# Kernel tuning notes

Hardware: AMD Instinct MI355X
Metric: run time of the kernel (lower is better)

Reference implementation:

```python
import jax, jax.numpy as jnp
import numpy as np

BS, OBJ, D = 32, 128, 256
R, E = 32, 64          # max_rels, relation_embedding_size
DEPTH = 3


def setup_inputs() -> dict:
    key = jax.random.key(0)
    ks = jax.random.split(key, 8)
    x = jax.random.normal(ks[0], (BS, OBJ, D), dtype=jnp.float32)
    # adjacency-style aggregation matrix [batch, objects, max_rels*objects]
    A = jax.random.uniform(ks[1], (BS, OBJ, R * OBJ), dtype=jnp.float32)
    rel_table = jax.random.normal(ks[2], (R, E), dtype=jnp.float32)
    # per-depth linear params (torch Linear y = x @ W^T + b; we store W already transposed to [in,out])
    s1 = 1.0 / np.sqrt(D)
    s2 = 1.0 / np.sqrt(D + E)
    W1 = jax.random.uniform(ks[3], (DEPTH, D, D), jnp.float32, -s1, s1)
    b1 = jax.random.uniform(ks[4], (DEPTH, D), jnp.float32, -s1, s1)
    W2 = jax.random.uniform(ks[5], (DEPTH, D + E, D), jnp.float32, -s2, s2)
    b2 = jax.random.uniform(ks[6], (DEPTH, D), jnp.float32, -s2, s2)
    return {"x": x, "A": A, "rel_table": rel_table, "W1": W1, "b1": b1, "W2": W2, "b2": b2}


def reference(x, A, rel_table, W1, b1, W2, b2):
    bs, o, d = x.shape
    r, e = rel_table.shape
    depth = W1.shape[0]
    # relation embeddings tiled per object (object-major, rel-minor): [o*r, e]
    rel = jnp.tile(rel_table, (o, 1))
    rel_b = jnp.broadcast_to(rel, (bs, o * r, e))
    for i in range(depth):
        # repeat each object's features over all relations: [bs, o*r, d]
        xr = jnp.repeat(x, r, axis=1)
        xr = jnp.concatenate([xr, rel_b], axis=-1)            # [bs, o*r, d+e]
        h1 = jnp.einsum('bod,df->bof', x, W1[i]) + b1[i]       # self transform
        h2 = jnp.einsum('bnc,cf->bnf', xr, W2[i]) + b2[i]      # relation-augmented transform
        agg = jnp.einsum('bon,bnf->bof', A, h2)                # bmm aggregate
        x = jnp.tanh(h1 + agg + x)                             # residual + tanh
    return x
```

## Files before the change

### kernel.cpp

```cpp
#include <hip/hip_runtime.h>
#include <math.h>

#define BS 32
#define OBJ 128
#define DD 256
#define RR 32
#define EE 64
#define NDEPTH 3

__global__ __launch_bounds__(256) void k_reduceA(const float* __restrict__ A,
                                                 float* __restrict__ Ao,
                                                 float* __restrict__ Ar,
                                                 float* __restrict__ As) {
    int wave = threadIdx.x >> 6;
    int lane = threadIdx.x & 63;
    int row  = blockIdx.x * 4 + wave;
    const float4* src = (const float4*)(A + (size_t)row * (RR * OBJ));
    float* AoRow = Ao + (size_t)row * OBJ;

    float4 arAcc = make_float4(0.f, 0.f, 0.f, 0.f);
#pragma unroll
    for (int it = 0; it < 16; ++it) {
        float4 v = src[it * 64 + lane];
        arAcc.x += v.x; arAcc.y += v.y; arAcc.z += v.z; arAcc.w += v.w;
        float s = v.x + v.y + v.z + v.w;
        s += __shfl_xor(s, 1);
        s += __shfl_xor(s, 2);
        s += __shfl_xor(s, 4);
        if ((lane & 7) == 0) AoRow[it * 8 + (lane >> 3)] = s;
    }
#pragma unroll
    for (int m = 8; m <= 32; m <<= 1) {
        arAcc.x += __shfl_xor(arAcc.x, m);
        arAcc.y += __shfl_xor(arAcc.y, m);
        arAcc.z += __shfl_xor(arAcc.z, m);
        arAcc.w += __shfl_xor(arAcc.w, m);
    }
    if (lane < 8) ((float4*)(Ar + (size_t)row * RR))[lane] = arAcc;
    float t = arAcc.x + arAcc.y + arAcc.z + arAcc.w;
    t += __shfl_xor(t, 1);
    t += __shfl_xor(t, 2);
    t += __shfl_xor(t, 4);
    if (lane == 0) As[row] = t;
}

__global__ __launch_bounds__(256) void k_rel(const float* __restrict__ rel,
                                             const float* __restrict__ W2,
                                             float* __restrict__ relpart) {
    int dr = blockIdx.x;
    int d = dr >> 5, r = dr & 31;
    int f = threadIdx.x;
    const float* w  = W2 + (size_t)d * (DD + EE) * DD + (size_t)DD * DD;
    const float* rl = rel + (size_t)r * EE;
    float acc = 0.f;
#pragma unroll 8
    for (int e = 0; e < EE; ++e)
        acc = fmaf(rl[e], w[(size_t)e * DD + f], acc);
    relpart[(size_t)dr * DD + f] = acc;
}

__global__ __launch_bounds__(256) void k_gemm1(const float* __restrict__ X,
                                               const float* __restrict__ W1,
                                               const float* __restrict__ W2,
                                               const float* __restrict__ b1,
                                               int d,
                                               float* __restrict__ h1,
                                               float* __restrict__ xw) {
    __shared__ float Xs[64][33];
    __shared__ float Ws[32][64];

    int m0 = blockIdx.y * 64;
    int n0blk = blockIdx.x * 64;
    bool isW1 = (n0blk < 256);
    int ncol0 = isW1 ? n0blk : (n0blk - 256);
    const float* Wbase = isW1 ? (W1 + (size_t)d * DD * DD)
                              : (W2 + (size_t)d * (DD + EE) * DD);

    int tid = threadIdx.x;
    int tx = tid & 15;
    int ty = tid >> 4;
    float acc[4][4] = {};

    for (int k0 = 0; k0 < 256; k0 += 32) {
#pragma unroll
        for (int i = 0; i < 2; ++i) {
            int idx = tid + 256 * i;
            int rrow = idx >> 3, c4 = idx & 7;
            float4 v = *(const float4*)(X + (size_t)(m0 + rrow) * DD + k0 + c4 * 4);
            Xs[rrow][c4 * 4 + 0] = v.x; Xs[rrow][c4 * 4 + 1] = v.y;
            Xs[rrow][c4 * 4 + 2] = v.z; Xs[rrow][c4 * 4 + 3] = v.w;
        }
#pragma unroll
        for (int i = 0; i < 2; ++i) {
            int idx = tid + 256 * i;
            int rrow = idx >> 4, c4 = idx & 15;
            *(float4*)(&Ws[rrow][c4 * 4]) =
                *(const float4*)(Wbase + (size_t)(k0 + rrow) * DD + ncol0 + c4 * 4);
        }
        __syncthreads();
#pragma unroll
        for (int kk = 0; kk < 32; ++kk) {
            float a0 = Xs[ty * 4 + 0][kk];
            float a1 = Xs[ty * 4 + 1][kk];
            float a2 = Xs[ty * 4 + 2][kk];
            float a3 = Xs[ty * 4 + 3][kk];
            float4 bv = *(const float4*)(&Ws[kk][tx * 4]);
            acc[0][0] = fmaf(a0, bv.x, acc[0][0]);
            acc[0][1] = fmaf(a0, bv.y, acc[0][1]);
            acc[0][2] = fmaf(a0, bv.z, acc[0][2]);
            acc[0][3] = fmaf(a0, bv.w, acc[0][3]);
            acc[1][0] = fmaf(a1, bv.x, acc[1][0]);
            acc[1][1] = fmaf(a1, bv.y, acc[1][1]);
            acc[1][2] = fmaf(a1, bv.z, acc[1][2]);
            acc[1][3] = fmaf(a1, bv.w, acc[1][3]);
            acc[2][0] = fmaf(a2, bv.x, acc[2][0]);
            acc[2][1] = fmaf(a2, bv.y, acc[2][1]);
            acc[2][2] = fmaf(a2, bv.z, acc[2][2]);
            acc[2][3] = fmaf(a2, bv.w, acc[2][3]);
            acc[3][0] = fmaf(a3, bv.x, acc[3][0]);
            acc[3][1] = fmaf(a3, bv.y, acc[3][1]);
            acc[3][2] = fmaf(a3, bv.z, acc[3][2]);
            acc[3][3] = fmaf(a3, bv.w, acc[3][3]);
        }
        __syncthreads();
    }

    float4 bias = make_float4(0.f, 0.f, 0.f, 0.f);
    if (isW1) bias = *(const float4*)(b1 + (size_t)d * DD + ncol0 + tx * 4);
    float* dst = isW1 ? h1 : xw;
#pragma unroll
    for (int i = 0; i < 4; ++i) {
        float4 o;
        o.x = acc[i][0] + bias.x;
        o.y = acc[i][1] + bias.y;
        o.z = acc[i][2] + bias.z;
        o.w = acc[i][3] + bias.w;
        *(float4*)(dst + (size_t)(m0 + ty * 4 + i) * DD + ncol0 + tx * 4) = o;
    }
}

__global__ __launch_bounds__(256) void k_agg(const float* __restrict__ Ao,
                                             const float* __restrict__ Ar,
                                             const float* __restrict__ As,
                                             const float* __restrict__ relpart,
                                             const float* __restrict__ b2,
                                             int d,
                                             const float* __restrict__ xw,
                                             const float* __restrict__ h1,
                                             const float* __restrict__ xin,
                                             float* __restrict__ xout) {
    __shared__ float Asm[64][33];
    __shared__ float Bs[32][64];

    int b  = blockIdx.z;
    int m0 = blockIdx.y * 64;
    int n0 = blockIdx.x * 64;
    int tid = threadIdx.x;
    int tx = tid & 15, ty = tid >> 4;

    const float* AoB = Ao + ((size_t)b * OBJ + m0) * OBJ;
    const float* ArB = Ar + ((size_t)b * OBJ + m0) * RR;
    const float* xwB = xw + (size_t)b * OBJ * DD;
    const float* rp  = relpart + (size_t)d * RR * DD;

    float acc[4][4] = {};

    for (int t = 0; t < 5; ++t) {
        if (t < 4) {
            int k0 = t * 32;
#pragma unroll
            for (int i = 0; i < 2; ++i) {
                int idx = tid + 256 * i;
                int rr = idx >> 3, c4 = idx & 7;
                float4 v = *(const float4*)(AoB + (size_t)rr * OBJ + k0 + c4 * 4);
                Asm[rr][c4 * 4 + 0] = v.x; Asm[rr][c4 * 4 + 1] = v.y;
                Asm[rr][c4 * 4 + 2] = v.z; Asm[rr][c4 * 4 + 3] = v.w;
            }
#pragma unroll
            for (int i = 0; i < 2; ++i) {
                int idx = tid + 256 * i;
                int rr = idx >> 4, c4 = idx & 15;
                *(float4*)(&Bs[rr][c4 * 4]) =
                    *(const float4*)(xwB + (size_t)(k0 + rr) * DD + n0 + c4 * 4);
            }
        } else {
#pragma unroll
            for (int i = 0; i < 2; ++i) {
                int idx = tid + 256 * i;
                int rr = idx >> 3, c4 = idx & 7;
                float4 v = *(const float4*)(ArB + (size_t)rr * RR + c4 * 4);
                Asm[rr][c4 * 4 + 0] = v.x; Asm[rr][c4 * 4 + 1] = v.y;
                Asm[rr][c4 * 4 + 2] = v.z; Asm[rr][c4 * 4 + 3] = v.w;
            }
#pragma unroll
            for (int i = 0; i < 2; ++i) {
                int idx = tid + 256 * i;
                int rr = idx >> 4, c4 = idx & 15;
                *(float4*)(&Bs[rr][c4 * 4]) =
                    *(const float4*)(rp + (size_t)rr * DD + n0 + c4 * 4);
            }
        }
        __syncthreads();
#pragma unroll
        for (int kk = 0; kk < 32; ++kk) {
            float a0 = Asm[ty * 4 + 0][kk];
            float a1 = Asm[ty * 4 + 1][kk];
            float a2 = Asm[ty * 4 + 2][kk];
            float a3 = Asm[ty * 4 + 3][kk];
            float4 bv = *(const float4*)(&Bs[kk][tx * 4]);
            acc[0][0] = fmaf(a0, bv.x, acc[0][0]);
            acc[0][1] = fmaf(a0, bv.y, acc[0][1]);
            acc[0][2] = fmaf(a0, bv.z, acc[0][2]);
            acc[0][3] = fmaf(a0, bv.w, acc[0][3]);
            acc[1][0] = fmaf(a1, bv.x, acc[1][0]);
            acc[1][1] = fmaf(a1, bv.y, acc[1][1]);
            acc[1][2] = fmaf(a1, bv.z, acc[1][2]);
            acc[1][3] = fmaf(a1, bv.w, acc[1][3]);
            acc[2][0] = fmaf(a2, bv.x, acc[2][0]);
            acc[2][1] = fmaf(a2, bv.y, acc[2][1]);
            acc[2][2] = fmaf(a2, bv.z, acc[2][2]);
            acc[2][3] = fmaf(a2, bv.w, acc[2][3]);
            acc[3][0] = fmaf(a3, bv.x, acc[3][0]);
            acc[3][1] = fmaf(a3, bv.y, acc[3][1]);
            acc[3][2] = fmaf(a3, bv.z, acc[3][2]);
            acc[3][3] = fmaf(a3, bv.w, acc[3][3]);
        }
        __syncthreads();
    }

    float4 b2v = *(const float4*)(b2 + (size_t)d * DD + n0 + tx * 4);
#pragma unroll
    for (int i = 0; i < 4; ++i) {
        int m = m0 + ty * 4 + i;
        float asv = As[(size_t)b * OBJ + m];
        size_t base = ((size_t)b * OBJ + m) * DD + n0 + tx * 4;
        float4 hv = *(const float4*)(h1 + base);
        float4 xv = *(const float4*)(xin + base);
        float4 o;
        o.x = tanhf(acc[i][0] + asv * b2v.x + hv.x + xv.x);
        o.y = tanhf(acc[i][1] + asv * b2v.y + hv.y + xv.y);
        o.z = tanhf(acc[i][2] + asv * b2v.z + hv.z + xv.z);
        o.w = tanhf(acc[i][3] + asv * b2v.w + hv.w + xv.w);
        *(float4*)(xout + base) = o;
    }
}

extern "C" void kernel_launch(void* const* d_in, const int* in_sizes, int n_in,
                              void* d_out, int out_size, void* d_ws, size_t ws_size,
                              hipStream_t stream) {
    const float* x    = (const float*)d_in[0];
    const float* A    = (const float*)d_in[1];
    const float* rel  = (const float*)d_in[2];
    const float* W1   = (const float*)d_in[3];
    const float* b1   = (const float*)d_in[4];
    const float* W2   = (const float*)d_in[5];
    const float* b2   = (const float*)d_in[6];
    float* out = (float*)d_out;

    float* Ao      = (float*)d_ws;
    float* Ar      = Ao + (size_t)BS * OBJ * OBJ;
    float* As_     = Ar + (size_t)BS * OBJ * RR;
    float* relpart = As_ + (size_t)BS * OBJ;
    float* xwbuf   = relpart + (size_t)NDEPTH * RR * DD;
    float* h1buf   = xwbuf + (size_t)BS * OBJ * DD;
    float* xbuf    = h1buf + (size_t)BS * OBJ * DD;

    k_reduceA<<<dim3(BS * OBJ / 4), dim3(256), 0, stream>>>(A, Ao, Ar, As_);
    k_rel<<<dim3(NDEPTH * RR), dim3(256), 0, stream>>>(rel, W2, relpart);

    const float* xcur = x;
    for (int d = 0; d < NDEPTH; ++d) {
        float* xnext = (d == NDEPTH - 1) ? out : xbuf;
        k_gemm1<<<dim3(8, 64), dim3(256), 0, stream>>>(xcur, W1, W2, b1, d, h1buf, xwbuf);
        k_agg<<<dim3(4, 2, BS), dim3(256), 0, stream>>>(Ao, Ar, As_, relpart, b2, d,
                                                        xwbuf, h1buf, xcur, xnext);
        xcur = xnext;
    }
}
```

Before: 214.6 us.

## Double-buffer shared tiles with register prefetch and transposed A layout in GEMM kernels

Both k_gemm1 and k_agg now stage tiles through registers into double-buffered shared memory. The next k-slice is loaded while the current one is computed, which leaves one barrier per iteration instead of two. The A/X operand is stored transposed so each thread reads a float4 of four rows per k step instead of four scalar loads. k_gemm1 also widens its tile to 64x128 (8 outputs per thread) and halves its grid, which raises register pressure and cuts the number of blocks to 256.

```diff
diff --git a/kernel.cpp b/kernel.cpp
--- a/kernel.cpp
+++ b/kernel.cpp
@@ -66,76 +66,109 @@
                                                int d,
                                                float* __restrict__ h1,
                                                float* __restrict__ xw) {
-    __shared__ float Xs[64][33];
-    __shared__ float Ws[32][64];
-
-    int m0 = blockIdx.y * 64;
-    int n0blk = blockIdx.x * 64;
-    bool isW1 = (n0blk < 256);
-    int ncol0 = isW1 ? n0blk : (n0blk - 256);
+    __shared__ float XT[2][32][68];
+    __shared__ float Ws[2][32][132];
+
+    const int m0 = blockIdx.y * 64;
+    const int n0blk = blockIdx.x * 128;
+    const bool isW1 = (n0blk < 256);
+    const int ncol0 = isW1 ? n0blk : (n0blk - 256);
     const float* Wbase = isW1 ? (W1 + (size_t)d * DD * DD)
                               : (W2 + (size_t)d * (DD + EE) * DD);
 
-    int tid = threadIdx.x;
-    int tx = tid & 15;
-    int ty = tid >> 4;
-    float acc[4][4] = {};
-
-    for (int k0 = 0; k0 < 256; k0 += 32) {
-#pragma unroll
-        for (int i = 0; i < 2; ++i) {
-            int idx = tid + 256 * i;
-            int rrow = idx >> 3, c4 = idx & 7;
-            float4 v = *(const float4*)(X + (size_t)(m0 + rrow) * DD + k0 + c4 * 4);
-            Xs[rrow][c4 * 4 + 0] = v.x; Xs[rrow][c4 * 4 + 1] = v.y;
-            Xs[rrow][c4 * 4 + 2] = v.z; Xs[rrow][c4 * 4 + 3] = v.w;
-        }
-#pragma unroll
-        for (int i = 0; i < 2; ++i) {
-            int idx = tid + 256 * i;
-            int rrow = idx >> 4, c4 = idx & 15;
-            *(float4*)(&Ws[rrow][c4 * 4]) =
-                *(const float4*)(Wbase + (size_t)(k0 + rrow) * DD + ncol0 + c4 * 4);
-        }
-        __syncthreads();
+    const int tid = threadIdx.x;
+    const int tx = tid & 15;
+    const int ty = tid >> 4;
+
+    const int xm0 = tid >> 3;
+    const int xc  = tid & 7;
+    const int wr0 = tid >> 5;
+    const int wc  = tid & 31;
+
+    float4 xr[2], wr4[4];
+    float acc0[4][4] = {};
+    float acc1[4][4] = {};
+
+#pragma unroll
+    for (int i = 0; i < 2; ++i)
+        xr[i] = *(const float4*)(X + (size_t)(m0 + xm0 + 32 * i) * DD + xc * 4);
+#pragma unroll
+    for (int i = 0; i < 4; ++i)
+        wr4[i] = *(const float4*)(Wbase + (size_t)(wr0 + 8 * i) * DD + ncol0 + wc * 4);
+#pragma unroll
+    for (int i = 0; i < 2; ++i) {
+        XT[0][xc * 4 + 0][xm0 + 32 * i] = xr[i].x;
+        XT[0][xc * 4 + 1][xm0 + 32 * i] = xr[i].y;
+        XT[0][xc * 4 + 2][xm0 + 32 * i] = xr[i].z;
+        XT[0][xc * 4 + 3][xm0 + 32 * i] = xr[i].w;
+    }
+#pragma unroll
+    for (int i = 0; i < 4; ++i)
+        *(float4*)(&Ws[0][wr0 + 8 * i][wc * 4]) = wr4[i];
+    __syncthreads();
+
+    for (int t = 0; t < 8; ++t) {
+        const int cur = t & 1;
+        if (t < 7) {
+            const int k0 = (t + 1) * 32;
+#pragma unroll
+            for (int i = 0; i < 2; ++i)
+                xr[i] = *(const float4*)(X + (size_t)(m0 + xm0 + 32 * i) * DD + k0 + xc * 4);
+#pragma unroll
+            for (int i = 0; i < 4; ++i)
+                wr4[i] = *(const float4*)(Wbase + (size_t)(k0 + wr0 + 8 * i) * DD + ncol0 + wc * 4);
+        }
 #pragma unroll
         for (int kk = 0; kk < 32; ++kk) {
-            float a0 = Xs[ty * 4 + 0][kk];
-            float a1 = Xs[ty * 4 + 1][kk];
-            float a2 = Xs[ty * 4 + 2][kk];
-            float a3 = Xs[ty * 4 + 3][kk];
-            float4 bv = *(const float4*)(&Ws[kk][tx * 4]);
-            acc[0][0] = fmaf(a0, bv.x, acc[0][0]);
-            acc[0][1] = fmaf(a0, bv.y, acc[0][1]);
-            acc[0][2] = fmaf(a0, bv.z, acc[0][2]);
-            acc[0][3] = fmaf(a0, bv.w, acc[0][3]);
-            acc[1][0] = fmaf(a1, bv.x, acc[1][0]);
-            acc[1][1] = fmaf(a1, bv.y, acc[1][1]);
-            acc[1][2] = fmaf(a1, bv.z, acc[1][2]);
-            acc[1][3] = fmaf(a1, bv.w, acc[1][3]);
-            acc[2][0] = fmaf(a2, bv.x, acc[2][0]);
-            acc[2][1] = fmaf(a2, bv.y, acc[2][1]);
-            acc[2][2] = fmaf(a2, bv.z, acc[2][2]);
-            acc[2][3] = fmaf(a2, bv.w, acc[2][3]);
-            acc[3][0] = fmaf(a3, bv.x, acc[3][0]);
-            acc[3][1] = fmaf(a3, bv.y, acc[3][1]);
-            acc[3][2] = fmaf(a3, bv.z, acc[3][2]);
-            acc[3][3] = fmaf(a3, bv.w, acc[3][3]);
-        }
-        __syncthreads();
-    }
-
-    float4 bias = make_float4(0.f, 0.f, 0.f, 0.f);
-    if (isW1) bias = *(const float4*)(b1 + (size_t)d * DD + ncol0 + tx * 4);
+            float4 a  = *(const float4*)(&XT[cur][kk][ty * 4]);
+            float4 b0 = *(const float4*)(&Ws[cur][kk][tx * 4]);
+            float4 b1v = *(const float4*)(&Ws[cur][kk][64 + tx * 4]);
+            const float am[4] = {a.x, a.y, a.z, a.w};
+#pragma unroll
+            for (int i = 0; i < 4; ++i) {
+                acc0[i][0] = fmaf(am[i], b0.x, acc0[i][0]);
+                acc0[i][1] = fmaf(am[i], b0.y, acc0[i][1]);
+                acc0[i][2] = fmaf(am[i], b0.z, acc0[i][2]);
+                acc0[i][3] = fmaf(am[i], b0.w, acc0[i][3]);
+                acc1[i][0] = fmaf(am[i], b1v.x, acc1[i][0]);
+                acc1[i][1] = fmaf(am[i], b1v.y, acc1[i][1]);
+                acc1[i][2] = fmaf(am[i], b1v.z, acc1[i][2]);
+                acc1[i][3] = fmaf(am[i], b1v.w, acc1[i][3]);
+            }
+        }
+        if (t < 7) {
+            const int nxt = cur ^ 1;
+#pragma unroll
+            for (int i = 0; i < 2; ++i) {
+                XT[nxt][xc * 4 + 0][xm0 + 32 * i] = xr[i].x;
+                XT[nxt][xc * 4 + 1][xm0 + 32 * i] = xr[i].y;
+                XT[nxt][xc * 4 + 2][xm0 + 32 * i] = xr[i].z;
+                XT[nxt][xc * 4 + 3][xm0 + 32 * i] = xr[i].w;
+            }
+#pragma unroll
+            for (int i = 0; i < 4; ++i)
+                *(float4*)(&Ws[nxt][wr0 + 8 * i][wc * 4]) = wr4[i];
+            __syncthreads();
+        }
+    }
+
+    float4 bias0 = make_float4(0.f, 0.f, 0.f, 0.f);
+    float4 bias1 = bias0;
+    if (isW1) {
+        bias0 = *(const float4*)(b1 + (size_t)d * DD + ncol0 + tx * 4);
+        bias1 = *(const float4*)(b1 + (size_t)d * DD + ncol0 + 64 + tx * 4);
+    }
     float* dst = isW1 ? h1 : xw;
 #pragma unroll
     for (int i = 0; i < 4; ++i) {
-        float4 o;
-        o.x = acc[i][0] + bias.x;
-        o.y = acc[i][1] + bias.y;
-        o.z = acc[i][2] + bias.z;
-        o.w = acc[i][3] + bias.w;
-        *(float4*)(dst + (size_t)(m0 + ty * 4 + i) * DD + ncol0 + tx * 4) = o;
+        size_t base = (size_t)(m0 + ty * 4 + i) * DD + ncol0;
+        float4 o0, o1;
+        o0.x = acc0[i][0] + bias0.x; o0.y = acc0[i][1] + bias0.y;
+        o0.z = acc0[i][2] + bias0.z; o0.w = acc0[i][3] + bias0.w;
+        o1.x = acc1[i][0] + bias1.x; o1.y = acc1[i][1] + bias1.y;
+        o1.z = acc1[i][2] + bias1.z; o1.w = acc1[i][3] + bias1.w;
+        *(float4*)(dst + base + tx * 4) = o0;
+        *(float4*)(dst + base + 64 + tx * 4) = o1;
     }
 }
 
@@ -149,83 +182,86 @@
                                              const float* __restrict__ h1,
                                              const float* __restrict__ xin,
                                              float* __restrict__ xout) {
-    __shared__ float Asm[64][33];
-    __shared__ float Bs[32][64];
-
-    int b  = blockIdx.z;
-    int m0 = blockIdx.y * 64;
-    int n0 = blockIdx.x * 64;
-    int tid = threadIdx.x;
-    int tx = tid & 15, ty = tid >> 4;
+    __shared__ float AT[2][32][68];
+    __shared__ float Bs[2][32][68];
+
+    const int b  = blockIdx.z;
+    const int m0 = blockIdx.y * 64;
+    const int n0 = blockIdx.x * 64;
+    const int tid = threadIdx.x;
+    const int tx = tid & 15, ty = tid >> 4;
 
     const float* AoB = Ao + ((size_t)b * OBJ + m0) * OBJ;
     const float* ArB = Ar + ((size_t)b * OBJ + m0) * RR;
     const float* xwB = xw + (size_t)b * OBJ * DD;
     const float* rp  = relpart + (size_t)d * RR * DD;
 
+    const int am0 = tid >> 3;
+    const int ac  = tid & 7;
+    const int br0 = tid >> 4;
+    const int bc  = tid & 15;
+
+    float4 areg[2], breg[2];
     float acc[4][4] = {};
 
+#pragma unroll
+    for (int i = 0; i < 2; ++i) {
+        areg[i] = *(const float4*)(AoB + (size_t)(am0 + 32 * i) * OBJ + ac * 4);
+        breg[i] = *(const float4*)(xwB + (size_t)(br0 + 16 * i) * DD + n0 + bc * 4);
+    }
+#pragma unroll
+    for (int i = 0; i < 2; ++i) {
+        AT[0][ac * 4 + 0][am0 + 32 * i] = areg[i].x;
+        AT[0][ac * 4 + 1][am0 + 32 * i] = areg[i].y;
+        AT[0][ac * 4 + 2][am0 + 32 * i] = areg[i].z;
+        AT[0][ac * 4 + 3][am0 + 32 * i] = areg[i].w;
+        *(float4*)(&Bs[0][br0 + 16 * i][bc * 4]) = breg[i];
+    }
+    __syncthreads();
+
     for (int t = 0; t < 5; ++t) {
+        const int cur = t & 1;
         if (t < 4) {
-            int k0 = t * 32;
+            if (t < 3) {
+                const int k0 = (t + 1) * 32;
+#pragma unroll
+                for (int i = 0; i < 2; ++i) {
+                    areg[i] = *(const float4*)(AoB + (size_t)(am0 + 32 * i) * OBJ + k0 + ac * 4);
+                    breg[i] = *(const float4*)(xwB + (size_t)(k0 + br0 + 16 * i) * DD + n0 + bc * 4);
+                }
+            } else {
+#pragma unroll
+                for (int i = 0; i < 2; ++i) {
+                    areg[i] = *(const float4*)(ArB + (size_t)(am0 + 32 * i) * RR + ac * 4);
+                    breg[i] = *(const float4*)(rp + (size_t)(br0 + 16 * i) * DD + n0 + bc * 4);
+                }
+            }
+        }
+#pragma unroll
+        for (int kk = 0; kk < 32; ++kk) {
+            float4 a = *(const float4*)(&AT[cur][kk][ty * 4]);
+            float4 bv = *(const float4*)(&Bs[cur][kk][tx * 4]);
+            const float am[4] = {a.x, a.y, a.z, a.w};
+#pragma unroll
+            for (int i = 0; i < 4; ++i) {
+                acc[i][0] = fmaf(am[i], bv.x, acc[i][0]);
+                acc[i][1] = fmaf(am[i], bv.y, acc[i][1]);
+                acc[i][2] = fmaf(am[i], bv.z, acc[i][2]);
+                acc[i][3] = fmaf(am[i], bv.w, acc[i][3]);
+            }
+        }
+        if (t < 4) {
+            const int nxt = cur ^ 1;
 #pragma unroll
             for (int i = 0; i < 2; ++i) {
-                int idx = tid + 256 * i;
-                int rr = idx >> 3, c4 = idx & 7;
-                float4 v = *(const float4*)(AoB + (size_t)rr * OBJ + k0 + c4 * 4);
-                Asm[rr][c4 * 4 + 0] = v.x; Asm[rr][c4 * 4 + 1] = v.y;
-                Asm[rr][c4 * 4 + 2] = v.z; Asm[rr][c4 * 4 + 3] = v.w;
-            }
-#pragma unroll
-            for (int i = 0; i < 2; ++i) {
-                int idx = tid + 256 * i;
-                int rr = idx >> 4, c4 = idx & 15;
-                *(float4*)(&Bs[rr][c4 * 4]) =
-                    *(const float4*)(xwB + (size_t)(k0 + rr) * DD + n0 + c4 * 4);
-            }
-        } else {
-#pragma unroll
-            for (int i = 0; i < 2; ++i) {
-                int idx = tid + 256 * i;
-                int rr = idx >> 3, c4 = idx & 7;
-                float4 v = *(const float4*)(ArB + (size_t)rr * RR + c4 * 4);
-                Asm[rr][c4 * 4 + 0] = v.x; Asm[rr][c4 * 4 + 1] = v.y;
-                Asm[rr][c4 * 4 + 2] = v.z; Asm[rr][c4 * 4 + 3] = v.w;
-            }
-#pragma unroll
-            for (int i = 0; i < 2; ++i) {
-                int idx = tid + 256 * i;
-                int rr = idx >> 4, c4 = idx & 15;
-                *(float4*)(&Bs[rr][c4 * 4]) =
-                    *(const float4*)(rp + (size_t)rr * DD + n0 + c4 * 4);
-            }
-        }
-        __syncthreads();
-#pragma unroll
-        for (int kk = 0; kk < 32; ++kk) {
-            float a0 = Asm[ty * 4 + 0][kk];
-            float a1 = Asm[ty * 4 + 1][kk];
-            float a2 = Asm[ty * 4 + 2][kk];
-            float a3 = Asm[ty * 4 + 3][kk];
-            float4 bv = *(const float4*)(&Bs[kk][tx * 4]);
-            acc[0][0] = fmaf(a0, bv.x, acc[0][0]);
-            acc[0][1] = fmaf(a0, bv.y, acc[0][1]);
-            acc[0][2] = fmaf(a0, bv.z, acc[0][2]);
-            acc[0][3] = fmaf(a0, bv.w, acc[0][3]);
-            acc[1][0] = fmaf(a1, bv.x, acc[1][0]);
-            acc[1][1] = fmaf(a1, bv.y, acc[1][1]);
-            acc[1][2] = fmaf(a1, bv.z, acc[1][2]);
-            acc[1][3] = fmaf(a1, bv.w, acc[1][3]);
-            acc[2][0] = fmaf(a2, bv.x, acc[2][0]);
-            acc[2][1] = fmaf(a2, bv.y, acc[2][1]);
-            acc[2][2] = fmaf(a2, bv.z, acc[2][2]);
-            acc[2][3] = fmaf(a2, bv.w, acc[2][3]);
-            acc[3][0] = fmaf(a3, bv.x, acc[3][0]);
-            acc[3][1] = fmaf(a3, bv.y, acc[3][1]);
-            acc[3][2] = fmaf(a3, bv.z, acc[3][2]);
-            acc[3][3] = fmaf(a3, bv.w, acc[3][3]);
-        }
-        __syncthreads();
+                AT[nxt][ac * 4 + 0][am0 + 32 * i] = areg[i].x;
+                AT[nxt][ac * 4 + 1][am0 + 32 * i] = areg[i].y;
+                AT[nxt][ac * 4 + 2][am0 + 32 * i] = areg[i].z;
+                AT[nxt][ac * 4 + 3][am0 + 32 * i] = areg[i].w;
+                *(float4*)(&Bs[nxt][br0 + 16 * i][bc * 4]) = breg[i];
+            }
+            __syncthreads();
+        }
     }
 
     float4 b2v = *(const float4*)(b2 + (size_t)d * DD + n0 + tx * 4);
@@ -271,7 +307,7 @@
     const float* xcur = x;
     for (int d = 0; d < NDEPTH; ++d) {
         float* xnext = (d == NDEPTH - 1) ? out : xbuf;
-        k_gemm1<<<dim3(8, 64), dim3(256), 0, stream>>>(xcur, W1, W2, b1, d, h1buf, xwbuf);
+        k_gemm1<<<dim3(4, 64), dim3(256), 0, stream>>>(xcur, W1, W2, b1, d, h1buf, xwbuf);
         k_agg<<<dim3(4, 2, BS), dim3(256), 0, stream>>>(Ao, Ar, As_, relpart, b2, d,
                                                         xwbuf, h1buf, xcur, xnext);
         xcur = xnext;
```

Result: slower. 258.4 us (+20.4%).

## Rewrite gemm1 as single-wave 8x8 register tile with double-buffered LDS

Applied to the files above, without the earlier changes.

The k_gemm1 tile GEMM now runs with 64 threads per block instead of 256, each computing an 8x8 output micro-tile, so fewer LDS reads are needed per FMA. Global loads for the next k-slice go into registers and are written to a second LDS buffer, which removes the __syncthreads barriers. The X tile uses an XOR-swizzled layout to avoid bank conflicts on float4 reads. With only 512 single-wave blocks, the GPU gets fewer waves to hide latency, and register pressure from 64 accumulators plus 16 prefetch float4s is high.

```diff
diff --git a/kernel.cpp b/kernel.cpp
--- a/kernel.cpp
+++ b/kernel.cpp
@@ -59,83 +59,108 @@
     relpart[(size_t)dr * DD + f] = acc;
 }
 
-__global__ __launch_bounds__(256) void k_gemm1(const float* __restrict__ X,
-                                               const float* __restrict__ W1,
-                                               const float* __restrict__ W2,
-                                               const float* __restrict__ b1,
-                                               int d,
-                                               float* __restrict__ h1,
-                                               float* __restrict__ xw) {
-    __shared__ float Xs[64][33];
-    __shared__ float Ws[32][64];
-
-    int m0 = blockIdx.y * 64;
-    int n0blk = blockIdx.x * 64;
-    bool isW1 = (n0blk < 256);
-    int ncol0 = isW1 ? n0blk : (n0blk - 256);
+__global__ __launch_bounds__(64) void k_gemm1(const float* __restrict__ X,
+                                              const float* __restrict__ W1,
+                                              const float* __restrict__ W2,
+                                              const float* __restrict__ b1,
+                                              int d,
+                                              float* __restrict__ h1,
+                                              float* __restrict__ xw) {
+    __shared__ float Xs[2][64][32];
+    __shared__ float Bs[2][32][68];
+
+    const int l  = threadIdx.x;
+    const int m0 = blockIdx.y * 64;
+    const int n0blk = blockIdx.x * 64;
+    const bool isW1 = (n0blk < 256);
+    const int ncol0 = isW1 ? n0blk : (n0blk - 256);
     const float* Wbase = isW1 ? (W1 + (size_t)d * DD * DD)
                               : (W2 + (size_t)d * (DD + EE) * DD);
 
-    int tid = threadIdx.x;
-    int tx = tid & 15;
-    int ty = tid >> 4;
-    float acc[4][4] = {};
-
-    for (int k0 = 0; k0 < 256; k0 += 32) {
-#pragma unroll
-        for (int i = 0; i < 2; ++i) {
-            int idx = tid + 256 * i;
-            int rrow = idx >> 3, c4 = idx & 7;
-            float4 v = *(const float4*)(X + (size_t)(m0 + rrow) * DD + k0 + c4 * 4);
-            Xs[rrow][c4 * 4 + 0] = v.x; Xs[rrow][c4 * 4 + 1] = v.y;
-            Xs[rrow][c4 * 4 + 2] = v.z; Xs[rrow][c4 * 4 + 3] = v.w;
-        }
-#pragma unroll
-        for (int i = 0; i < 2; ++i) {
-            int idx = tid + 256 * i;
-            int rrow = idx >> 4, c4 = idx & 15;
-            *(float4*)(&Ws[rrow][c4 * 4]) =
-                *(const float4*)(Wbase + (size_t)(k0 + rrow) * DD + ncol0 + c4 * 4);
-        }
-        __syncthreads();
-#pragma unroll
-        for (int kk = 0; kk < 32; ++kk) {
-            float a0 = Xs[ty * 4 + 0][kk];
-            float a1 = Xs[ty * 4 + 1][kk];
-            float a2 = Xs[ty * 4 + 2][kk];
-            float a3 = Xs[ty * 4 + 3][kk];
-            float4 bv = *(const float4*)(&Ws[kk][tx * 4]);
-            acc[0][0] = fmaf(a0, bv.x, acc[0][0]);
-            acc[0][1] = fmaf(a0, bv.y, acc[0][1]);
-            acc[0][2] = fmaf(a0, bv.z, acc[0][2]);
-            acc[0][3] = fmaf(a0, bv.w, acc[0][3]);
-            acc[1][0] = fmaf(a1, bv.x, acc[1][0]);
-            acc[1][1] = fmaf(a1, bv.y, acc[1][1]);
-            acc[1][2] = fmaf(a1, bv.z, acc[1][2]);
-            acc[1][3] = fmaf(a1, bv.w, acc[1][3]);
-            acc[2][0] = fmaf(a2, bv.x, acc[2][0]);
-            acc[2][1] = fmaf(a2, bv.y, acc[2][1]);
-            acc[2][2] = fmaf(a2, bv.z, acc[2][2]);
-            acc[2][3] = fmaf(a2, bv.w, acc[2][3]);
-            acc[3][0] = fmaf(a3, bv.x, acc[3][0]);
-            acc[3][1] = fmaf(a3, bv.y, acc[3][1]);
-            acc[3][2] = fmaf(a3, bv.z, acc[3][2]);
-            acc[3][3] = fmaf(a3, bv.w, acc[3][3]);
-        }
-        __syncthreads();
-    }
-
-    float4 bias = make_float4(0.f, 0.f, 0.f, 0.f);
-    if (isW1) bias = *(const float4*)(b1 + (size_t)d * DD + ncol0 + tx * 4);
+    const int tx = l & 7;
+    const int ty = l >> 3;
+
+    const int ar_ = l >> 3, ac_ = l & 7;
+    const int br_ = l >> 4, bc_ = l & 15;
+    const float* aG = X + (size_t)(m0 + ar_) * DD + ac_ * 4;
+    const float* bG = Wbase + (size_t)br_ * DD + ncol0 + bc_ * 4;
+
+    float4 pa[8], pb[8];
+    float acc[8][8] = {};
+
+#pragma unroll
+    for (int j = 0; j < 8; ++j)
+        pa[j] = *(const float4*)(aG + (size_t)(8 * j) * DD);
+#pragma unroll
+    for (int j = 0; j < 8; ++j)
+        pb[j] = *(const float4*)(bG + (size_t)(4 * j) * DD);
+#pragma unroll
+    for (int j = 0; j < 8; ++j)
+        *(float4*)&Xs[0][ar_ + 8 * j][((ac_ ^ j) & 7) * 4] = pa[j];
+#pragma unroll
+    for (int j = 0; j < 8; ++j)
+        *(float4*)&Bs[0][br_ + 4 * j][bc_ * 4] = pb[j];
+
+    for (int t = 0; t < 8; ++t) {
+        const int cur = t & 1;
+        if (t < 7) {
+            const int k0n = (t + 1) * 32;
+#pragma unroll
+            for (int j = 0; j < 8; ++j)
+                pa[j] = *(const float4*)(aG + (size_t)(8 * j) * DD + k0n);
+#pragma unroll
+            for (int j = 0; j < 8; ++j)
+                pb[j] = *(const float4*)(bG + (size_t)(k0n + 4 * j) * DD);
+        }
+#pragma unroll
+        for (int g = 0; g < 8; ++g) {
+            float4 af[8];
+#pragma unroll
+            for (int i = 0; i < 8; ++i)
+                af[i] = *(const float4*)&Xs[cur][ty * 8 + i][((g ^ ty) & 7) * 4];
+#pragma unroll
+            for (int k2 = 0; k2 < 4; ++k2) {
+                float4 b0  = *(const float4*)&Bs[cur][g * 4 + k2][tx * 8];
+                float4 b1v = *(const float4*)&Bs[cur][g * 4 + k2][tx * 8 + 4];
+                const float bb[8] = {b0.x, b0.y, b0.z, b0.w,
+                                     b1v.x, b1v.y, b1v.z, b1v.w};
+#pragma unroll
+                for (int i = 0; i < 8; ++i) {
+                    const float av = ((const float*)&af[i])[k2];
+#pragma unroll
+                    for (int jj = 0; jj < 8; ++jj)
+                        acc[i][jj] = fmaf(av, bb[jj], acc[i][jj]);
+                }
+            }
+        }
+        if (t < 7) {
+            const int nxt = cur ^ 1;
+#pragma unroll
+            for (int j = 0; j < 8; ++j)
+                *(float4*)&Xs[nxt][ar_ + 8 * j][((ac_ ^ j) & 7) * 4] = pa[j];
+#pragma unroll
+            for (int j = 0; j < 8; ++j)
+                *(float4*)&Bs[nxt][br_ + 4 * j][bc_ * 4] = pb[j];
+        }
+    }
+
+    float4 bias0 = make_float4(0.f, 0.f, 0.f, 0.f);
+    float4 bias1 = bias0;
+    if (isW1) {
+        bias0 = *(const float4*)(b1 + (size_t)d * DD + ncol0 + tx * 8);
+        bias1 = *(const float4*)(b1 + (size_t)d * DD + ncol0 + tx * 8 + 4);
+    }
     float* dst = isW1 ? h1 : xw;
 #pragma unroll
-    for (int i = 0; i < 4; ++i) {
-        float4 o;
-        o.x = acc[i][0] + bias.x;
-        o.y = acc[i][1] + bias.y;
-        o.z = acc[i][2] + bias.z;
-        o.w = acc[i][3] + bias.w;
-        *(float4*)(dst + (size_t)(m0 + ty * 4 + i) * DD + ncol0 + tx * 4) = o;
+    for (int i = 0; i < 8; ++i) {
+        size_t base = (size_t)(m0 + ty * 8 + i) * DD + ncol0 + tx * 8;
+        float4 o0, o1;
+        o0.x = acc[i][0] + bias0.x; o0.y = acc[i][1] + bias0.y;
+        o0.z = acc[i][2] + bias0.z; o0.w = acc[i][3] + bias0.w;
+        o1.x = acc[i][4] + bias1.x; o1.y = acc[i][5] + bias1.y;
+        o1.z = acc[i][6] + bias1.z; o1.w = acc[i][7] + bias1.w;
+        *(float4*)(dst + base) = o0;
+        *(float4*)(dst + base + 4) = o1;
     }
 }
 
@@ -152,11 +177,11 @@
     __shared__ float Asm[64][33];
     __shared__ float Bs[32][64];
 
-    int b  = blockIdx.z;
-    int m0 = blockIdx.y * 64;
-    int n0 = blockIdx.x * 64;
-    int tid = threadIdx.x;
-    int tx = tid & 15, ty = tid >> 4;
+    const int b  = blockIdx.z;
+    const int m0 = blockIdx.y * 64;
+    const int n0 = blockIdx.x * 64;
+    const int tid = threadIdx.x;
+    const int tx = tid & 15, ty = tid >> 4;
 
     const float* AoB = Ao + ((size_t)b * OBJ + m0) * OBJ;
     const float* ArB = Ar + ((size_t)b * OBJ + m0) * RR;
@@ -167,7 +192,7 @@
 
     for (int t = 0; t < 5; ++t) {
         if (t < 4) {
-            int k0 = t * 32;
+            const int k0 = t * 32;
 #pragma unroll
             for (int i = 0; i < 2; ++i) {
                 int idx = tid + 256 * i;
@@ -271,7 +296,7 @@
     const float* xcur = x;
     for (int d = 0; d < NDEPTH; ++d) {
         float* xnext = (d == NDEPTH - 1) ? out : xbuf;
-        k_gemm1<<<dim3(8, 64), dim3(256), 0, stream>>>(xcur, W1, W2, b1, d, h1buf, xwbuf);
+        k_gemm1<<<dim3(8, 64), dim3(64), 0, stream>>>(xcur, W1, W2, b1, d, h1buf, xwbuf);
         k_agg<<<dim3(4, 2, BS), dim3(256), 0, stream>>>(Ao, Ar, As_, relpart, b2, d,
                                                         xwbuf, h1buf, xcur, xnext);
         xcur = xnext;
```

After: 389.0 us. +81.2%, slower.
